# Performance work log

Measured on AMD Instinct MI355X. Metric: run time of the kernel, lower is better.

Reference implementation:

```python
import jax, jax.numpy as jnp
import numpy as np


def setup_inputs() -> dict:
    key = jax.random.key(0)
    k1, k2 = jax.random.split(key)
    B, T, D = 32, 512, 512
    x = jax.random.normal(k1, (B, T, D), dtype=jnp.float32)
    duration = jax.random.randint(k2, (B, T), 0, 8, dtype=jnp.int32)
    return {"x": x, "duration": duration, "max_len": 2048}


def reference(x, duration, max_len):
    """Vectorized length regulator.

    x:        [B, T, D] float
    duration: [B, T] int frames per phoneme
    max_len:  static python int, padded output length

    Returns (output [B, max_len, D], mel_lengths [B]).
    Frame t of sample b copies phoneme j where j is the first index with
    cumsum(duration)[b, j] > t (i.e. searchsorted right). Frames beyond the
    total duration are zero-padded; sequences longer than max_len are truncated
    (mel_lengths reports the untruncated length, matching the torch module,
    with the all-zero-duration edge case yielding length 1).
    """
    B, T, D = x.shape
    csum = jnp.cumsum(duration, axis=1)            # [B, T]
    dur_sum = csum[:, -1]                          # [B]
    t = jnp.arange(max_len, dtype=csum.dtype)      # [max_len]
    # phoneme index for each output frame: searchsorted(csum[b], t, 'right')
    idx = jax.vmap(lambda c: jnp.searchsorted(c, t, side='right'))(csum)  # [B, max_len]
    idx = jnp.clip(idx, 0, T - 1)
    out = jnp.take_along_axis(x, idx[:, :, None], axis=1)  # [B, max_len, D]
    valid = t[None, :] < dur_sum[:, None]                  # [B, max_len]
    out = jnp.where(valid[:, :, None], out, jnp.zeros((), dtype=x.dtype))
    mel_lengths = jnp.maximum(dur_sum, 1).astype(jnp.int32)
    return out, mel_lengths
```

## Files before the change

kernel.cpp:

```cpp
#include <hip/hip_runtime.h>


#define BB      32
#define TT      512
#define DD      512
#define MAXLEN  2048
#define CHUNK   64
#define NCHUNK  (MAXLEN / CHUNK)

typedef float f4 __attribute__((ext_vector_type(4)));

__global__ __launch_bounds__(512) void lr_fused_kernel(
    const int* __restrict__ dur, const f4* __restrict__ x,
    f4* __restrict__ out, float* __restrict__ mel_out) {
  __shared__ int s[TT];
  __shared__ int s_idx[CHUNK];

  const int b     = blockIdx.x >> 5;
  const int chunk = blockIdx.x & (NCHUNK - 1);
  const int tid   = threadIdx.x;

  s[tid] = dur[b * TT + tid];
  __syncthreads();
#pragma unroll
  for (int off = 1; off < TT; off <<= 1) {
    int v = (tid >= off) ? s[tid - off] : 0;
    __syncthreads();
    s[tid] += v;
    __syncthreads();
  }
  const int dsum = s[TT - 1];
  if (chunk == 0 && tid == 0) {
    mel_out[b] = (float)(dsum > 1 ? dsum : 1);
  }

  const int base = chunk * CHUNK;
  if (tid < CHUNK) {
    int t = base + tid;
    int v = -1;
    if (t < dsum) {
      int lo = 0, hi = TT;
      while (lo < hi) {
        int mid = (lo + hi) >> 1;
        if (s[mid] <= t) lo = mid + 1; else hi = mid;
      }
      v = lo < (TT - 1) ? lo : (TT - 1);
    }
    s_idx[tid] = v;
  }
  __syncthreads();

  const int lane = tid & 127;
  const int fsub = tid >> 7;
  const f4 zero = {0.f, 0.f, 0.f, 0.f};
#pragma unroll
  for (int it = 0; it < 16; ++it) {
    const int f = it * 4 + fsub;
    const int idx = s_idx[f];
    f4 v = zero;
    if (idx >= 0) {
      v = x[((size_t)b * TT + idx) * (DD / 4) + lane];
    }
    __builtin_nontemporal_store(
        v, &out[((size_t)b * MAXLEN + base + f) * (DD / 4) + lane]);
  }
}

extern "C" void kernel_launch(void* const* d_in, const int* in_sizes, int n_in,
                              void* d_out, int out_size, void* d_ws, size_t ws_size,
                              hipStream_t stream) {
  const float* x   = (const float*)d_in[0];
  const int*   dur = (const int*)d_in[1];
  float* out = (float*)d_out;
  float* mel_out = out + (size_t)BB * MAXLEN * DD;

  lr_fused_kernel<<<BB * NCHUNK, 512, 0, stream>>>(
      dur, (const f4*)x, (f4*)out, mel_out);
}
```

Baseline: 173.1 us.

## Use wave-shuffle scan for cumsum and double frames per block

The shared-memory Hillis-Steele prefix sum, which needed two barriers per step, becomes a 64-lane shuffle scan plus a small cross-wave fixup with two barriers. The frames handled per block go from 64 to 128, halving the number of blocks and so the redundant per-block cumsum work. The copy loop is now partially unrolled by 8 instead of fully unrolled. The risk is fewer blocks giving less parallelism, though 512 blocks should still fill the device.

```diff
diff --git a/kernel.cpp b/kernel.cpp
--- a/kernel.cpp
+++ b/kernel.cpp
@@ -5,7 +5,7 @@
 #define TT      512
 #define DD      512
 #define MAXLEN  2048
-#define CHUNK   64
+#define CHUNK   128
 #define NCHUNK  (MAXLEN / CHUNK)
 
 typedef float f4 __attribute__((ext_vector_type(4)));
@@ -14,21 +14,29 @@
     const int* __restrict__ dur, const f4* __restrict__ x,
     f4* __restrict__ out, float* __restrict__ mel_out) {
   __shared__ int s[TT];
+  __shared__ int wsum[8];
   __shared__ int s_idx[CHUNK];
 
-  const int b     = blockIdx.x >> 5;
+  const int b     = blockIdx.x >> 4;
   const int chunk = blockIdx.x & (NCHUNK - 1);
   const int tid   = threadIdx.x;
+  const int lane  = tid & 63;
+  const int wave  = tid >> 6;
 
-  s[tid] = dur[b * TT + tid];
+  int v = dur[b * TT + tid];
+#pragma unroll
+  for (int off = 1; off < 64; off <<= 1) {
+    int u = __shfl_up(v, off, 64);
+    if (lane >= off) v += u;
+  }
+  if (lane == 63) wsum[wave] = v;
   __syncthreads();
+  int add = 0;
 #pragma unroll
-  for (int off = 1; off < TT; off <<= 1) {
-    int v = (tid >= off) ? s[tid - off] : 0;
-    __syncthreads();
-    s[tid] += v;
-    __syncthreads();
-  }
+  for (int w = 0; w < 7; ++w) add += (w < wave) ? wsum[w] : 0;
+  s[tid] = v + add;
+  __syncthreads();
+
   const int dsum = s[TT - 1];
   if (chunk == 0 && tid == 0) {
     mel_out[b] = (float)(dsum > 1 ? dsum : 1);
@@ -37,32 +45,32 @@
   const int base = chunk * CHUNK;
   if (tid < CHUNK) {
     int t = base + tid;
-    int v = -1;
+    int r = -1;
     if (t < dsum) {
       int lo = 0, hi = TT;
       while (lo < hi) {
         int mid = (lo + hi) >> 1;
         if (s[mid] <= t) lo = mid + 1; else hi = mid;
       }
-      v = lo < (TT - 1) ? lo : (TT - 1);
+      r = lo < (TT - 1) ? lo : (TT - 1);
     }
-    s_idx[tid] = v;
+    s_idx[tid] = r;
   }
   __syncthreads();
 
-  const int lane = tid & 127;
+  const int l4   = tid & 127;
   const int fsub = tid >> 7;
   const f4 zero = {0.f, 0.f, 0.f, 0.f};
-#pragma unroll
-  for (int it = 0; it < 16; ++it) {
+#pragma unroll 8
+  for (int it = 0; it < CHUNK / 4; ++it) {
     const int f = it * 4 + fsub;
     const int idx = s_idx[f];
-    f4 v = zero;
+    f4 val = zero;
     if (idx >= 0) {
-      v = x[((size_t)b * TT + idx) * (DD / 4) + lane];
+      val = x[((size_t)b * TT + idx) * (DD / 4) + l4];
     }
     __builtin_nontemporal_store(
-        v, &out[((size_t)b * MAXLEN + base + f) * (DD / 4) + lane]);
+        val, &out[((size_t)b * MAXLEN + base + f) * (DD / 4) + l4]);
   }
 }
 
```

Measured after the change: 174.2 us. About the same (+0.7%).
